# Performance work log

Hardware: AMD Instinct MI355X
Metric: run time of the kernel (lower is better)

## Reference

```python
import jax, jax.numpy as jnp
import numpy as np

V, D, DFF, E, K, L = 32000, 1024, 4096, 8, 2, 2
B, S = 2, 1024


def _layer_norm(x, scale, bias, eps=1e-5):
    mu = jnp.mean(x, axis=-1, keepdims=True)
    var = jnp.var(x, axis=-1, keepdims=True)
    return (x - mu) * jax.lax.rsqrt(var + eps) * scale + bias


def setup_inputs() -> dict:
    key = jax.random.key(0)
    ks = jax.random.split(key, 16)
    s = 0.02
    return {
        "input_ids": jax.random.randint(ks[0], (B, S), 0, V, dtype=jnp.int32),
        "emb": jax.random.normal(ks[1], (V, D), jnp.float32) * s,
        "t_ln_scale": jnp.ones((L, D), jnp.float32),
        "t_ln_bias": jnp.zeros((L, D), jnp.float32),
        "t_w1": jax.random.normal(ks[2], (L, D, DFF), jnp.float32) * s,
        "t_b1": jnp.zeros((L, DFF), jnp.float32),
        "t_w2": jax.random.normal(ks[3], (L, DFF, D), jnp.float32) * s,
        "t_b2": jnp.zeros((L, D), jnp.float32),
        "Wr": jax.random.normal(ks[4], (D, E), jnp.float32) * s,
        "br": jnp.zeros((E,), jnp.float32),
        "e_w1": jax.random.normal(ks[5], (E, D, DFF), jnp.float32) * s,
        "e_b1": jnp.zeros((E, DFF), jnp.float32),
        "e_w2": jax.random.normal(ks[6], (E, DFF, D), jnp.float32) * s,
        "e_b2": jnp.zeros((E, D), jnp.float32),
        "Wl": jax.random.normal(ks[7], (D, V), jnp.float32) * s,
        "bl": jnp.zeros((V,), jnp.float32),
    }


def reference(input_ids, emb, t_ln_scale, t_ln_bias, t_w1, t_b1, t_w2, t_b2,
              Wr, br, e_w1, e_b1, e_w2, e_b2, Wl, bl):
    # token embeddings: [B,S,D]
    x = emb[input_ids]

    # temporal abstraction: L pre-LN residual MLP blocks
    for l in range(L):
        h = _layer_norm(x, t_ln_scale[l], t_ln_bias[l])
        h = jax.nn.gelu(jnp.einsum('bsd,df->bsf', h, t_w1[l]) + t_b1[l])
        x = x + jnp.einsum('bsf,fd->bsd', h, t_w2[l]) + t_b2[l]

    # router: top-k renormalized softmax over experts, scattered to [B,S,E]
    r_logits = jnp.einsum('bsd,de->bse', x, Wr) + br
    top_vals, top_idx = jax.lax.top_k(r_logits, K)
    top_w = jax.nn.softmax(top_vals, axis=-1)
    routing_weights = jnp.put_along_axis(
        jnp.zeros_like(r_logits), top_idx, top_w, axis=-1, inplace=False)

    # dense all-experts stack: [B,S,E,D]
    h = jax.nn.gelu(jnp.einsum('bsd,edf->bsef', x, e_w1) + e_b1)
    expert_out = jnp.einsum('bsef,efd->bsed', h, e_w2) + e_b2

    # sparse-weighted combine
    y = jnp.einsum('bse,bsed->bsd', routing_weights, expert_out)

    logits = jnp.einsum('bsd,dv->bsv', y, Wl) + bl
    return logits, routing_weights
```

## Files before the change

### kernel.cpp

```cpp
#include <hip/hip_runtime.h>
#include <stdint.h>

typedef __bf16 bf16;
typedef __bf16 bf16x8 __attribute__((ext_vector_type(8)));
typedef float f32x4 __attribute__((ext_vector_type(4)));

#define DEV __device__ __forceinline__

static constexpr int Dm   = 1024;
static constexpr int DFFm = 4096;
static constexpr int Tm   = 2048;
static constexpr int Vm   = 32000;

#define GLOAD_LDS16(g, l)                                                      \
  __builtin_amdgcn_global_load_lds(                                            \
      (const __attribute__((address_space(1))) unsigned int*)(g),              \
      (__attribute__((address_space(3))) unsigned int*)(l), 16, 0, 0)

DEV float gelu_fast(float v) {
  float u = 0.7978845608028654f * (v + 0.044715f * v * v * v);
  float e = __expf(2.0f * u);
  float t = 1.0f - 2.0f / (e + 1.0f);
  return 0.5f * v * (1.0f + t);
}
DEV float gelu_precise(float v) {
  float u = 0.7978845608028654f * (v + 0.044715f * v * v * v);
  return 0.5f * v * (1.0f + tanhf(u));
}

enum { EPI_GELU_SPLIT = 0, EPI_RESID = 1, EPI_GELU_BF16 = 2, EPI_MOE = 3, EPI_BIAS = 4 };

struct GemmP {
  const bf16* Ah;
  const bf16* Bh;
  const float* bias;
  const float* rwp;
  const int* cnt;
  const int* idx;
  float* outF;
  bf16* outH;
  int K; int N;
  int lda; int ldb; int ldo;
  long aBS, bBS, outBS;
  int biasBS;
  int ebase;
};

template <int EPI, bool GATHER, bool SWZ>
__launch_bounds__(256, 2)
__global__ void gemm_bt(GemmP p) {
  constexpr bool SPARSE = GATHER || (EPI == EPI_MOE);
  __shared__ bf16 lds[8192];
  bf16* ldsA = lds;
  bf16* ldsB = lds + 4096;

  const int tid  = threadIdx.x;
  const int lane = tid & 63;
  const int wid  = tid >> 6;
  const int wr   = wid >> 1;
  const int wc   = wid & 1;
  const int z    = blockIdx.z;

  int bx = blockIdx.x, by = blockIdx.y;
  if constexpr (SWZ) {
    const int gx = gridDim.x, gy = gridDim.y;
    const int nwg = gx * gy;
    const int lin = by * gx + bx;
    const int q = nwg >> 3, r = nwg & 7;
    const int xcd = lin & 7, loc = lin >> 3;
    const int nid = (xcd < r ? xcd * (q + 1) : r * (q + 1) + (xcd - r) * q) + loc;
    bx = nid / gy; by = nid % gy;
  }

  const long am0 = (long)by * 128;
  const long bn0 = (long)bx * 128;

  int cntE = 0;
  const int* il = nullptr;
  if constexpr (SPARSE) {
    cntE = p.cnt[p.ebase + z];
    if (am0 >= cntE) return;
    il = p.idx + (long)(p.ebase + z) * 2048;
  }

  const long lda = p.lda, ldb = p.ldb;
  const long K = p.K;

  const int c0 = wid * 64 + lane;
  const int c1 = 256 + wid * 64 + lane;
  const bf16 *aS0, *aS1, *bS0, *bS1;
  {
    const bf16* Bb = p.Bh + (long)z * p.bBS + bn0 * ldb;
    bS0 = Bb + (long)(c0 >> 2) * ldb + (c0 & 3) * 8;
    bS1 = Bb + (long)(c1 >> 2) * ldb + (c1 & 3) * 8;
    if constexpr (GATHER) {
      const int g0 = (int)am0 + (c0 >> 2);
      const int g1 = (int)am0 + (c1 >> 2);
      const long r0 = il[g0 < cntE ? g0 : 0];
      const long r1 = il[g1 < cntE ? g1 : 0];
      aS0 = p.Ah + r0 * lda + (c0 & 3) * 8;
      aS1 = p.Ah + r1 * lda + (c1 & 3) * 8;
    } else {
      const bf16* Ab = p.Ah + (long)z * p.aBS + am0 * lda;
      aS0 = Ab + (long)(c0 >> 2) * lda + (c0 & 3) * 8;
      aS1 = Ab + (long)(c1 >> 2) * lda + (c1 & 3) * 8;
    }
  }
  char* dst0 = (char*)(void*)lds + (wid * 64) * 16;
  char* dst1 = (char*)(void*)lds + (256 + wid * 64) * 16;

  f32x4 acc[4][4] = {};

  const int aoff = (wr * 64 + (lane & 15)) * 32 + (lane >> 4) * 8;
  const int boff = (wc * 64 + (lane & 15)) * 32 + (lane >> 4) * 8;

  for (long k0 = 0; k0 < K; k0 += 32) {
    __syncthreads();
    GLOAD_LDS16(aS0 + k0, dst0);
    GLOAD_LDS16(aS1 + k0, dst1);
    GLOAD_LDS16(bS0 + k0, dst0 + 8192);
    GLOAD_LDS16(bS1 + k0, dst1 + 8192);
    __syncthreads();

    bf16x8 a[4], b[4];
#pragma unroll
    for (int m = 0; m < 4; ++m) a[m] = *(const bf16x8*)(ldsA + aoff + m * 512);
#pragma unroll
    for (int n = 0; n < 4; ++n) b[n] = *(const bf16x8*)(ldsB + boff + n * 512);
#pragma unroll
    for (int m = 0; m < 4; ++m)
#pragma unroll
      for (int n = 0; n < 4; ++n)
        acc[m][n] = __builtin_amdgcn_mfma_f32_16x16x32_bf16(a[m], b[n], acc[m][n], 0, 0, 0);
  }

  const long N = p.N;

#pragma unroll
  for (int m = 0; m < 4; ++m) {
#pragma unroll
    for (int n = 0; n < 4; ++n) {
      const long col = bn0 + wc * 64 + n * 16 + (lane & 15);
      float bv;
      if constexpr (EPI == EPI_RESID) bv = (z == 0) ? p.bias[col] : 0.0f;
      else bv = p.bias[(long)z * p.biasBS + col];
#pragma unroll
      for (int r = 0; r < 4; ++r) {
        const long row = am0 + wr * 64 + m * 16 + (lane >> 4) * 4 + r;
        float v = acc[m][n][r] + bv;
        if constexpr (EPI == EPI_GELU_SPLIT) {
          float g = gelu_precise(v);
          bf16 h = (bf16)g;
          long o = row * (long)p.ldo + col;
          p.outH[o] = h;
          p.outH[o + N] = (bf16)(g - (float)h);
          p.outH[o + 2 * N] = h;
        } else if constexpr (EPI == EPI_RESID) {
          atomicAdd(p.outF + row * N + col, v);
        } else if constexpr (EPI == EPI_GELU_BF16) {
          long o = (long)z * p.outBS + row * N + col;
          p.outH[o] = (bf16)gelu_fast(v);
        } else if constexpr (EPI == EPI_MOE) {
          if (row < cntE) {
            const int tok = il[row];
            const float wgt = p.rwp[(long)tok * 8 + p.ebase + z];
            atomicAdd(p.outF + (long)tok * N + col, wgt * v);
          }
        } else {
          __builtin_nontemporal_store(v, p.outF + row * N + col);
        }
      }
    }
  }
}

template <bool AUG>
__global__ void transpose_cvt(const float* __restrict__ in, bf16* __restrict__ out,
                              int R, int C, long inBS, long outBS) {
  __shared__ float tile[32][33];
  const float* inp = in + (long)blockIdx.z * inBS;
  const long c0 = (long)blockIdx.x * 32;
  const long r0 = (long)blockIdx.y * 32;
  const int tx = threadIdx.x;
  const int ty = threadIdx.y;
#pragma unroll
  for (int i = 0; i < 4; ++i) {
    int r = ty + i * 8;
    tile[r][tx] = inp[(r0 + r) * (long)C + c0 + tx];
  }
  __syncthreads();
  const long ob = (long)blockIdx.z * outBS;
  const long stride = AUG ? 3L * R : (long)R;
#pragma unroll
  for (int i = 0; i < 4; ++i) {
    int c = ty + i * 8;
    float v = tile[tx][c];
    bf16 h = (bf16)v;
    long o = ob + (c0 + c) * stride + r0 + tx;
    out[o] = h;
    if constexpr (AUG) {
      out[o + R] = h;
      out[o + 2 * R] = (bf16)(v - (float)h);
    }
  }
}

__global__ void embed_kernel(const int* __restrict__ ids, const float* __restrict__ emb,
                             float* __restrict__ x) {
  const long t = blockIdx.x;
  const int id = ids[t];
  ((float4*)(x + t * 1024))[threadIdx.x] = ((const float4*)(emb + (long)id * 1024))[threadIdx.x];
}

__global__ void ln_aug_kernel(const float* __restrict__ x, const float* __restrict__ sc,
                              const float* __restrict__ bi, bf16* __restrict__ oa) {
  const long t = blockIdx.x;
  const int tid = threadIdx.x;
  const int lane = tid & 63, wid = tid >> 6;
  float4 a = ((const float4*)(x + t * 1024))[tid];
  float s = a.x + a.y + a.z + a.w;
  float q = a.x * a.x + a.y * a.y + a.z * a.z + a.w * a.w;
#pragma unroll
  for (int off = 32; off; off >>= 1) {
    s += __shfl_down(s, off);
    q += __shfl_down(q, off);
  }
  __shared__ float sr[4], qr[4];
  if (lane == 0) { sr[wid] = s; qr[wid] = q; }
  __syncthreads();
  s = sr[0] + sr[1] + sr[2] + sr[3];
  q = qr[0] + qr[1] + qr[2] + qr[3];
  const float mu = s * (1.0f / 1024.0f);
  const float var = q * (1.0f / 1024.0f) - mu * mu;
  const float rs = rsqrtf(var + 1e-5f);
#pragma unroll
  for (int j = 0; j < 4; ++j) {
    const int d = tid * 4 + j;
    const float g = (((const float*)&a)[j] - mu) * rs * sc[d] + bi[d];
    const bf16 h = (bf16)g;
    oa[t * 3072 + d] = h;
    oa[t * 3072 + 1024 + d] = (bf16)(g - (float)h);
    oa[t * 3072 + 2048 + d] = h;
  }
}

__global__ void router_kernel(const float* __restrict__ x, const float* __restrict__ Wr,
                              const float* __restrict__ br, float* __restrict__ rwo,
                              int* __restrict__ top2) {
  const long t = blockIdx.x;
  const int lane = threadIdx.x;
  float acc[8];
#pragma unroll
  for (int e = 0; e < 8; ++e) acc[e] = 0.0f;
  const float4* xr = (const float4*)(x + t * 1024);
#pragma unroll
  for (int j = 0; j < 4; ++j) {
    const int d4 = j * 64 + lane;
    float4 xv = xr[d4];
#pragma unroll
    for (int u = 0; u < 4; ++u) {
      const float xs = ((const float*)&xv)[u];
      const float4* wp = (const float4*)(Wr + (long)(d4 * 4 + u) * 8);
      float4 w0 = wp[0], w1 = wp[1];
      acc[0] += xs * w0.x; acc[1] += xs * w0.y; acc[2] += xs * w0.z; acc[3] += xs * w0.w;
      acc[4] += xs * w1.x; acc[5] += xs * w1.y; acc[6] += xs * w1.z; acc[7] += xs * w1.w;
    }
  }
#pragma unroll
  for (int off = 32; off; off >>= 1)
#pragma unroll
    for (int e = 0; e < 8; ++e) acc[e] += __shfl_down(acc[e], off);
  if (lane == 0) {
    float v[8];
#pragma unroll
    for (int e = 0; e < 8; ++e) v[e] = acc[e] + br[e];
    int i0 = 0; float v0 = v[0];
    for (int e = 1; e < 8; ++e) if (v[e] > v0) { v0 = v[e]; i0 = e; }
    int i1 = -1; float v1 = -3.4e38f;
    for (int e = 0; e < 8; ++e) if (e != i0 && v[e] > v1) { v1 = v[e]; i1 = e; }
    float e1 = expf(v1 - v0);
    float den = 1.0f + e1;
    float w0 = 1.0f / den, w1 = e1 / den;
    float* o = rwo + t * 8;
#pragma unroll
    for (int e = 0; e < 8; ++e) o[e] = (e == i0) ? w0 : (e == i1 ? w1 : 0.0f);
    top2[t] = i0 | (i1 << 8);
  }
}

__global__ void build_lists(const int* __restrict__ top2, int* __restrict__ cnt,
                            int* __restrict__ idx) {
  const int t = blockIdx.x * 256 + threadIdx.x;
  const int rec = top2[t];
  const int e0 = rec & 255, e1 = (rec >> 8) & 255;
  int p0 = atomicAdd(&cnt[e0], 1);
  idx[e0 * 2048 + p0] = t;
  int p1 = atomicAdd(&cnt[e1], 1);
  idx[e1 * 2048 + p1] = t;
}

__global__ void cvt_bf16_kernel(const float* __restrict__ in, bf16* __restrict__ out, long n) {
  long i = ((long)blockIdx.x * blockDim.x + threadIdx.x) * 8;
  if (i >= n) return;
  float4 a = *(const float4*)(in + i);
  float4 b = *(const float4*)(in + i + 4);
  bf16x8 o;
  o[0] = (bf16)a.x; o[1] = (bf16)a.y; o[2] = (bf16)a.z; o[3] = (bf16)a.w;
  o[4] = (bf16)b.x; o[5] = (bf16)b.y; o[6] = (bf16)b.z; o[7] = (bf16)b.w;
  *(bf16x8*)(out + i) = o;
}

extern "C" void kernel_launch(void* const* d_in, const int* in_sizes, int n_in,
                              void* d_out, int out_size, void* d_ws, size_t ws_size,
                              hipStream_t stream) {
  (void)in_sizes; (void)n_in; (void)out_size; (void)ws_size;
  const int*   ids  = (const int*)d_in[0];
  const float* emb  = (const float*)d_in[1];
  const float* tlns = (const float*)d_in[2];
  const float* tlnb = (const float*)d_in[3];
  const float* tw1  = (const float*)d_in[4];
  const float* tb1  = (const float*)d_in[5];
  const float* tw2  = (const float*)d_in[6];
  const float* tb2  = (const float*)d_in[7];
  const float* Wr   = (const float*)d_in[8];
  const float* br   = (const float*)d_in[9];
  const float* ew1  = (const float*)d_in[10];
  const float* eb1  = (const float*)d_in[11];
  const float* ew2  = (const float*)d_in[12];
  const float* eb2  = (const float*)d_in[13];
  const float* Wl   = (const float*)d_in[14];
  const float* bl   = (const float*)d_in[15];

  float* logits = (float*)d_out;
  float* rwout  = (float*)d_out + (long)Tm * Vm;

  size_t off = 0;
  auto take = [&](size_t bytes) {
    void* pp = (char*)d_ws + off;
    off += (bytes + 255) & ~(size_t)255;
    return pp;
  };
  float* X    = (float*)take((size_t)Tm * Dm * 4);
  bf16*  XB   = (bf16*) take((size_t)Tm * Dm * 2);
  float* Y    = (float*)take((size_t)Tm * Dm * 4);
  bf16*  YB   = (bf16*) take((size_t)Tm * Dm * 2);
  int*   top2 = (int*)  take((size_t)Tm * 4);
  int*   cnt  = (int*)  take(8 * 4);
  int*   idxl = (int*)  take((size_t)8 * Tm * 4);
  char*  S    = (char*) take(134217728);

  bf16* A1  = (bf16*)S;
  bf16* W1A = (bf16*)(S + 12582912);
  bf16* W2A = (bf16*)(S + 12582912 + 25165824);
  bf16* HTA = (bf16*)(S + 12582912 + 2 * 25165824);
  bf16* EW1T = (bf16*)S;
  bf16* HE   = (bf16*)(S + 33554432);
  bf16* EW2T = (bf16*)(S + 100663296);
  bf16* WLT  = (bf16*)S;

  embed_kernel<<<dim3(Tm), dim3(256), 0, stream>>>(ids, emb, X);

  for (int l = 0; l < 2; ++l) {
    transpose_cvt<true><<<dim3(DFFm / 32, Dm / 32, 1), dim3(32, 8), 0, stream>>>(
        tw1 + (long)l * Dm * DFFm, W1A, Dm, DFFm, 0, 0);
    transpose_cvt<true><<<dim3(Dm / 32, DFFm / 32, 1), dim3(32, 8), 0, stream>>>(
        tw2 + (long)l * DFFm * Dm, W2A, DFFm, Dm, 0, 0);
    ln_aug_kernel<<<dim3(Tm), dim3(256), 0, stream>>>(X, tlns + l * Dm, tlnb + l * Dm, A1);

    GemmP p1{};
    p1.Ah = A1; p1.Bh = W1A;
    p1.bias = tb1 + (long)l * DFFm;
    p1.outH = HTA;
    p1.K = 3072; p1.N = DFFm; p1.lda = 3072; p1.ldb = 3072; p1.ldo = 3 * DFFm;
    gemm_bt<EPI_GELU_SPLIT, false, true>
        <<<dim3(DFFm / 128, Tm / 128, 1), dim3(256), 0, stream>>>(p1);

    GemmP p2{};
    p2.Ah = HTA; p2.Bh = W2A;
    p2.bias = tb2 + (long)l * Dm;
    p2.outF = X;
    p2.K = 6144; p2.N = Dm; p2.lda = 12288; p2.ldb = 12288;
    p2.aBS = 6144; p2.bBS = 6144;
    gemm_bt<EPI_RESID, false, true>
        <<<dim3(Dm / 128, Tm / 128, 2), dim3(256), 0, stream>>>(p2);
  }

  router_kernel<<<dim3(Tm), dim3(64), 0, stream>>>(X, Wr, br, rwout, top2);
  hipMemsetAsync(cnt, 0, 8 * 4, stream);
  build_lists<<<dim3(Tm / 256), dim3(256), 0, stream>>>(top2, cnt, idxl);
  cvt_bf16_kernel<<<dim3(Tm * Dm / (256 * 8)), dim3(256), 0, stream>>>(X, XB, (long)Tm * Dm);
  hipMemsetAsync(Y, 0, (size_t)Tm * Dm * 4, stream);

  for (int q = 0; q < 2; ++q) {
    transpose_cvt<false><<<dim3(DFFm / 32, Dm / 32, 4), dim3(32, 8), 0, stream>>>(
        ew1 + (long)q * 4 * Dm * DFFm, EW1T, Dm, DFFm, (long)Dm * DFFm, (long)DFFm * Dm);
    transpose_cvt<false><<<dim3(Dm / 32, DFFm / 32, 4), dim3(32, 8), 0, stream>>>(
        ew2 + (long)q * 4 * DFFm * Dm, EW2T, DFFm, Dm, (long)DFFm * Dm, (long)Dm * DFFm);

    GemmP pe1{};
    pe1.Ah = XB; pe1.Bh = EW1T;
    pe1.bias = eb1 + (long)q * 4 * DFFm; pe1.biasBS = DFFm;
    pe1.outH = HE; pe1.outBS = (long)Tm * DFFm;
    pe1.aBS = 0; pe1.bBS = (long)DFFm * Dm;
    pe1.cnt = cnt; pe1.idx = idxl; pe1.ebase = q * 4;
    pe1.K = Dm; pe1.N = DFFm; pe1.lda = Dm; pe1.ldb = Dm;
    gemm_bt<EPI_GELU_BF16, true, true>
        <<<dim3(DFFm / 128, Tm / 128, 4), dim3(256), 0, stream>>>(pe1);

    GemmP pe2{};
    pe2.Ah = HE; pe2.aBS = (long)Tm * DFFm;
    pe2.Bh = EW2T; pe2.bBS = (long)Dm * DFFm;
    pe2.bias = eb2 + (long)q * 4 * Dm; pe2.biasBS = Dm;
    pe2.rwp = rwout; pe2.cnt = cnt; pe2.idx = idxl; pe2.ebase = q * 4;
    pe2.outF = Y;
    pe2.K = DFFm; pe2.N = Dm; pe2.lda = DFFm; pe2.ldb = DFFm;
    gemm_bt<EPI_MOE, false, true>
        <<<dim3(Dm / 128, Tm / 128, 4), dim3(256), 0, stream>>>(pe2);
  }

  cvt_bf16_kernel<<<dim3(Tm * Dm / (256 * 8)), dim3(256), 0, stream>>>(Y, YB, (long)Tm * Dm);
  transpose_cvt<false><<<dim3(Vm / 32, Dm / 32, 1), dim3(32, 8), 0, stream>>>(
      Wl, WLT, Dm, Vm, 0, 0);
  GemmP pl{};
  pl.Ah = YB; pl.Bh = WLT; pl.bias = bl;
  pl.outF = logits;
  pl.K = Dm; pl.N = Vm; pl.lda = Dm; pl.ldb = Dm;
  gemm_bt<EPI_BIAS, false, true>
      <<<dim3(Vm / 128, Tm / 128, 1), dim3(256), 0, stream>>>(pl);
}
```

Measured before the change: 1.192 ms.

## Double K-tile to 64 with XOR-swizzled LDS and add split-K for down GEMMs

The GEMM kernel now stages 64-wide K tiles with an XOR-swizzled LDS layout, so each barrier pair covers twice the MFMA work and LDS bank conflicts drop. A generic split-K index (kcShift/kcK) is added. The temporal down-projection is split 8 ways and the expert down-projection 4 ways, with partial sums combined through the existing atomic epilogues to raise grid parallelism. The split-GELU epilogue switches from tanhf to the exp-based approximation, and the logits store no longer uses nontemporal stores. Costs are more atomic traffic, doubled LDS per block (which may lower occupancy), and slightly different GELU numerics.

```diff
diff --git a/kernel.cpp b/kernel.cpp
--- a/kernel.cpp
+++ b/kernel.cpp
@@ -17,15 +17,11 @@
       (const __attribute__((address_space(1))) unsigned int*)(g),              \
       (__attribute__((address_space(3))) unsigned int*)(l), 16, 0, 0)
 
-DEV float gelu_fast(float v) {
+DEV float gelu_tanh(float v) {
   float u = 0.7978845608028654f * (v + 0.044715f * v * v * v);
   float e = __expf(2.0f * u);
   float t = 1.0f - 2.0f / (e + 1.0f);
   return 0.5f * v * (1.0f + t);
-}
-DEV float gelu_precise(float v) {
-  float u = 0.7978845608028654f * (v + 0.044715f * v * v * v);
-  return 0.5f * v * (1.0f + tanhf(u));
 }
 
 enum { EPI_GELU_SPLIT = 0, EPI_RESID = 1, EPI_GELU_BF16 = 2, EPI_MOE = 3, EPI_BIAS = 4 };
@@ -44,15 +40,15 @@
   long aBS, bBS, outBS;
   int biasBS;
   int ebase;
+  int kcShift; int kcK;
 };
 
 template <int EPI, bool GATHER, bool SWZ>
 __launch_bounds__(256, 2)
 __global__ void gemm_bt(GemmP p) {
-  constexpr bool SPARSE = GATHER || (EPI == EPI_MOE);
-  __shared__ bf16 lds[8192];
+  __shared__ bf16 lds[16384];
   bf16* ldsA = lds;
-  bf16* ldsB = lds + 4096;
+  bf16* ldsB = lds + 8192;
 
   const int tid  = threadIdx.x;
   const int lane = tid & 63;
@@ -60,6 +56,8 @@
   const int wr   = wid >> 1;
   const int wc   = wid & 1;
   const int z    = blockIdx.z;
+  const int kc   = z & ((1 << p.kcShift) - 1);
+  const int ze   = z >> p.kcShift;
 
   int bx = blockIdx.x, by = blockIdx.y;
   if constexpr (SWZ) {
@@ -77,61 +75,71 @@
 
   int cntE = 0;
   const int* il = nullptr;
-  if constexpr (SPARSE) {
-    cntE = p.cnt[p.ebase + z];
+  if constexpr (GATHER || EPI == EPI_MOE) {
+    cntE = p.cnt[p.ebase + ze];
     if (am0 >= cntE) return;
-    il = p.idx + (long)(p.ebase + z) * 2048;
+    il = p.idx + (long)(p.ebase + ze) * 2048;
   }
 
   const long lda = p.lda, ldb = p.ldb;
   const long K = p.K;
-
-  const int c0 = wid * 64 + lane;
-  const int c1 = 256 + wid * 64 + lane;
-  const bf16 *aS0, *aS1, *bS0, *bS1;
+  const long kco = (long)kc * p.kcK;
+
+  const int sub = (lane & 7) ^ (lane >> 3);
+  const int rIn = wid * 8 + (lane >> 3);
+
+  const bf16 *aS[4], *bS[4];
   {
-    const bf16* Bb = p.Bh + (long)z * p.bBS + bn0 * ldb;
-    bS0 = Bb + (long)(c0 >> 2) * ldb + (c0 & 3) * 8;
-    bS1 = Bb + (long)(c1 >> 2) * ldb + (c1 & 3) * 8;
-    if constexpr (GATHER) {
-      const int g0 = (int)am0 + (c0 >> 2);
-      const int g1 = (int)am0 + (c1 >> 2);
-      const long r0 = il[g0 < cntE ? g0 : 0];
-      const long r1 = il[g1 < cntE ? g1 : 0];
-      aS0 = p.Ah + r0 * lda + (c0 & 3) * 8;
-      aS1 = p.Ah + r1 * lda + (c1 & 3) * 8;
-    } else {
-      const bf16* Ab = p.Ah + (long)z * p.aBS + am0 * lda;
-      aS0 = Ab + (long)(c0 >> 2) * lda + (c0 & 3) * 8;
-      aS1 = Ab + (long)(c1 >> 2) * lda + (c1 & 3) * 8;
-    }
-  }
-  char* dst0 = (char*)(void*)lds + (wid * 64) * 16;
-  char* dst1 = (char*)(void*)lds + (256 + wid * 64) * 16;
+    const bf16* Bb = p.Bh + (long)ze * p.bBS + kco + bn0 * ldb;
+    const bf16* Ab = p.Ah + (long)ze * p.aBS + kco + am0 * lda;
+#pragma unroll
+    for (int j = 0; j < 4; ++j) {
+      const int row = j * 32 + rIn;
+      bS[j] = Bb + (long)row * ldb + sub * 8;
+      if constexpr (GATHER) {
+        const int rt = (int)am0 + row;
+        const long grow = il[rt < cntE ? rt : 0];
+        aS[j] = p.Ah + grow * lda + kco + sub * 8;
+      } else {
+        aS[j] = Ab + (long)row * lda + sub * 8;
+      }
+    }
+  }
+  char* dstA[4];
+#pragma unroll
+  for (int j = 0; j < 4; ++j)
+    dstA[j] = (char*)(void*)lds + (j * 256 + wid * 64) * 16;
 
   f32x4 acc[4][4] = {};
 
-  const int aoff = (wr * 64 + (lane & 15)) * 32 + (lane >> 4) * 8;
-  const int boff = (wc * 64 + (lane & 15)) * 32 + (lane >> 4) * 8;
-
-  for (long k0 = 0; k0 < K; k0 += 32) {
+  const int r15 = lane & 15;
+  const int kcs = lane >> 4;
+  const int xk  = lane & 7;
+
+  for (long k0 = 0; k0 < K; k0 += 64) {
     __syncthreads();
-    GLOAD_LDS16(aS0 + k0, dst0);
-    GLOAD_LDS16(aS1 + k0, dst1);
-    GLOAD_LDS16(bS0 + k0, dst0 + 8192);
-    GLOAD_LDS16(bS1 + k0, dst1 + 8192);
+#pragma unroll
+    for (int j = 0; j < 4; ++j) {
+      GLOAD_LDS16(aS[j] + k0, dstA[j]);
+      GLOAD_LDS16(bS[j] + k0, dstA[j] + 16384);
+    }
     __syncthreads();
-
-    bf16x8 a[4], b[4];
-#pragma unroll
-    for (int m = 0; m < 4; ++m) a[m] = *(const bf16x8*)(ldsA + aoff + m * 512);
-#pragma unroll
-    for (int n = 0; n < 4; ++n) b[n] = *(const bf16x8*)(ldsB + boff + n * 512);
-#pragma unroll
-    for (int m = 0; m < 4; ++m)
+#pragma unroll
+    for (int h = 0; h < 2; ++h) {
+      const int q8 = ((kcs + 4 * h) ^ xk) << 3;
+      bf16x8 a[4], b[4];
+#pragma unroll
+      for (int m = 0; m < 4; ++m)
+        a[m] = *(const bf16x8*)(ldsA + (wr * 64 + m * 16 + r15) * 64 + q8);
 #pragma unroll
       for (int n = 0; n < 4; ++n)
-        acc[m][n] = __builtin_amdgcn_mfma_f32_16x16x32_bf16(a[m], b[n], acc[m][n], 0, 0, 0);
+        b[n] = *(const bf16x8*)(ldsB + (wc * 64 + n * 16 + r15) * 64 + q8);
+#pragma unroll
+      for (int m = 0; m < 4; ++m)
+#pragma unroll
+        for (int n = 0; n < 4; ++n)
+          acc[m][n] = __builtin_amdgcn_mfma_f32_16x16x32_bf16(a[m], b[n], acc[m][n], 0, 0, 0);
+    }
   }
 
   const long N = p.N;
@@ -141,33 +149,31 @@
 #pragma unroll
     for (int n = 0; n < 4; ++n) {
       const long col = bn0 + wc * 64 + n * 16 + (lane & 15);
-      float bv;
-      if constexpr (EPI == EPI_RESID) bv = (z == 0) ? p.bias[col] : 0.0f;
-      else bv = p.bias[(long)z * p.biasBS + col];
+      const float bv = (kc == 0) ? p.bias[(long)ze * p.biasBS + col] : 0.0f;
 #pragma unroll
       for (int r = 0; r < 4; ++r) {
         const long row = am0 + wr * 64 + m * 16 + (lane >> 4) * 4 + r;
         float v = acc[m][n][r] + bv;
         if constexpr (EPI == EPI_GELU_SPLIT) {
-          float g = gelu_precise(v);
-          bf16 h = (bf16)g;
+          float g = gelu_tanh(v);
+          bf16 hh = (bf16)g;
           long o = row * (long)p.ldo + col;
-          p.outH[o] = h;
-          p.outH[o + N] = (bf16)(g - (float)h);
-          p.outH[o + 2 * N] = h;
+          p.outH[o] = hh;
+          p.outH[o + N] = (bf16)(g - (float)hh);
+          p.outH[o + 2 * N] = hh;
         } else if constexpr (EPI == EPI_RESID) {
           atomicAdd(p.outF + row * N + col, v);
         } else if constexpr (EPI == EPI_GELU_BF16) {
-          long o = (long)z * p.outBS + row * N + col;
-          p.outH[o] = (bf16)gelu_fast(v);
+          long o = (long)ze * p.outBS + row * N + col;
+          p.outH[o] = (bf16)gelu_tanh(v);
         } else if constexpr (EPI == EPI_MOE) {
           if (row < cntE) {
             const int tok = il[row];
-            const float wgt = p.rwp[(long)tok * 8 + p.ebase + z];
+            const float wgt = p.rwp[(long)tok * 8 + p.ebase + ze];
             atomicAdd(p.outF + (long)tok * N + col, wgt * v);
           }
         } else {
-          __builtin_nontemporal_store(v, p.outF + row * N + col);
+          p.outF[row * N + col] = v;
         }
       }
     }
@@ -379,10 +385,10 @@
     p2.Ah = HTA; p2.Bh = W2A;
     p2.bias = tb2 + (long)l * Dm;
     p2.outF = X;
-    p2.K = 6144; p2.N = Dm; p2.lda = 12288; p2.ldb = 12288;
-    p2.aBS = 6144; p2.bBS = 6144;
+    p2.K = 1536; p2.N = Dm; p2.lda = 12288; p2.ldb = 12288;
+    p2.kcShift = 3; p2.kcK = 1536;
     gemm_bt<EPI_RESID, false, true>
-        <<<dim3(Dm / 128, Tm / 128, 2), dim3(256), 0, stream>>>(p2);
+        <<<dim3(Dm / 128, Tm / 128, 8), dim3(256), 0, stream>>>(p2);
   }
 
   router_kernel<<<dim3(Tm), dim3(64), 0, stream>>>(X, Wr, br, rwout, top2);
@@ -413,9 +419,10 @@
     pe2.bias = eb2 + (long)q * 4 * Dm; pe2.biasBS = Dm;
     pe2.rwp = rwout; pe2.cnt = cnt; pe2.idx = idxl; pe2.ebase = q * 4;
     pe2.outF = Y;
-    pe2.K = DFFm; pe2.N = Dm; pe2.lda = DFFm; pe2.ldb = DFFm;
+    pe2.K = 1024; pe2.N = Dm; pe2.lda = DFFm; pe2.ldb = DFFm;
+    pe2.kcShift = 2; pe2.kcK = 1024;
     gemm_bt<EPI_MOE, false, true>
-        <<<dim3(Dm / 128, Tm / 128, 4), dim3(256), 0, stream>>>(pe2);
+        <<<dim3(Dm / 128, Tm / 128, 16), dim3(256), 0, stream>>>(pe2);
   }
 
   cvt_bf16_kernel<<<dim3(Tm * Dm / (256 * 8)), dim3(256), 0, stream>>>(Y, YB, (long)Tm * Dm);
```

Result: faster. 1.007 ms (-15.5%).
